# Kernel optimization log

Measured on AMD Instinct MI355X. Metric: run time of the kernel, lower is better.

Reference implementation:

```python
import jax, jax.numpy as jnp
import numpy as np


def setup_inputs() -> dict:
    key = jax.random.key(0)
    k1, k2, k3, k4 = jax.random.split(key, 4)
    N, F, E = 131072, 512, 256
    x = jax.random.normal(k1, (N, F), dtype=jnp.float32)
    W = jax.random.normal(k2, (E, F), dtype=jnp.float32) * 0.05  # stacked weak-classifier weights
    b = jax.random.normal(k3, (E,), dtype=jnp.float32) * 0.05
    alphas = jax.random.normal(k4, (E,), dtype=jnp.float32)
    return {"x": x, "W": W, "b": b, "alphas": alphas}


def reference(x, W, b, alphas):
    # Fused version of the per-estimator Python loop:
    # per estimator e: pred_e = round(sigmoid(x @ W[e] + b[e])) in {0,1}
    logits = jnp.einsum('nf,ef->ne', x, W) + b              # [N, E]
    preds = jnp.round(jax.nn.sigmoid(logits))               # [N, E], half-to-even like torch.round
    # original casts each (alpha * pred) term to long (trunc toward zero) before accumulating
    terms = jnp.trunc(alphas[None, :] * preds)              # [N, E]
    acc = jnp.sum(terms, axis=1)                            # [N]
    return jnp.sign(acc)
```

## Files before the change

kernel.cpp:

```cpp
#include <hip/hip_runtime.h>
#include <math.h>


#define BM 128
#define BN 128
#define BK 16
#define TAU 2e-4f
#define F_DIM 512

__device__ __attribute__((noinline)) bool exact_pred(const float* __restrict__ xr,
                                                     const float* __restrict__ wr,
                                                     float bv) {
    double s = (double)bv;
    for (int k = 0; k < F_DIM; ++k)
        s = fma((double)xr[k], (double)wr[k], s);
    return s > 0.0;
}

__global__ __launch_bounds__(256)
void ada_fused(const float* __restrict__ x, const float* __restrict__ W,
               const float* __restrict__ bias, const float* __restrict__ alphas,
               float* __restrict__ out) {
    __shared__ float xs[BK][BM];
    __shared__ float wsh[BK][BN];
    __shared__ int   rowacc[BM];
    __shared__ int   se[256];
    __shared__ float st[256];
    __shared__ float sb[256];
    __shared__ int   wcnt[4];

    const int tid = threadIdx.x;
    const int n0  = blockIdx.x * BM;

    se[tid] = 0; st[tid] = 0.0f; sb[tid] = 0.0f;
    if (tid < BM) rowacc[tid] = 0;
    __syncthreads();

    const float t = truncf(alphas[tid]);
    const bool flag = (t != 0.0f);
    const unsigned long long mask = __ballot(flag);
    const int lane = tid & 63, wv = tid >> 6;
    if (lane == 0) wcnt[wv] = __popcll(mask);
    __syncthreads();
    int off = 0;
    #pragma unroll
    for (int w = 0; w < 4; ++w)
        if (w < wv) off += wcnt[w];
    const int M = wcnt[0] + wcnt[1] + wcnt[2] + wcnt[3];
    if (flag) {
        const int slot = off + __popcll(mask & ((1ull << lane) - 1ull));
        se[slot] = tid;
        st[slot] = t;
        sb[slot] = bias[tid];
    }
    __syncthreads();

    const int ttx = tid & 15, tty = tid >> 4;
    const int row0 = ttx * 8, col0 = tty * 8;
    const int lr = tid >> 1;
    const int lk = (tid & 1) * 8;

    for (int cb = 0; cb < M; cb += BN) {
        const bool active = (cb + col0) < M;
        const int serow = se[cb + lr];
        const float4* xp = (const float4*)(x + (size_t)(n0 + lr) * F_DIM + lk);
        const float4* wp = (const float4*)(W + (size_t)serow * F_DIM + lk);

        float acc[8][8];
        #pragma unroll
        for (int r = 0; r < 8; ++r)
            #pragma unroll
            for (int c = 0; c < 8; ++c) acc[r][c] = 0.0f;

        for (int k0 = 0; k0 < F_DIM; k0 += BK) {
            const float4 xa = xp[0], xb = xp[1];
            const float4 wa = wp[0], wb = wp[1];
            xp += BK / 4; wp += BK / 4;
            __syncthreads();
            xs[lk + 0][lr] = xa.x; xs[lk + 1][lr] = xa.y;
            xs[lk + 2][lr] = xa.z; xs[lk + 3][lr] = xa.w;
            xs[lk + 4][lr] = xb.x; xs[lk + 5][lr] = xb.y;
            xs[lk + 6][lr] = xb.z; xs[lk + 7][lr] = xb.w;
            wsh[lk + 0][lr] = wa.x; wsh[lk + 1][lr] = wa.y;
            wsh[lk + 2][lr] = wa.z; wsh[lk + 3][lr] = wa.w;
            wsh[lk + 4][lr] = wb.x; wsh[lk + 5][lr] = wb.y;
            wsh[lk + 6][lr] = wb.z; wsh[lk + 7][lr] = wb.w;
            __syncthreads();
            if (active) {
                #pragma unroll
                for (int kk = 0; kk < BK; ++kk) {
                    float a[8], w8[8];
                    *(float4*)&a[0]  = *(const float4*)&xs[kk][row0];
                    *(float4*)&a[4]  = *(const float4*)&xs[kk][row0 + 4];
                    *(float4*)&w8[0] = *(const float4*)&wsh[kk][col0];
                    *(float4*)&w8[4] = *(const float4*)&wsh[kk][col0 + 4];
                    #pragma unroll
                    for (int r = 0; r < 8; ++r)
                        #pragma unroll
                        for (int c = 0; c < 8; ++c)
                            acc[r][c] = fmaf(a[r], w8[c], acc[r][c]);
                }
            }
        }

        if (active) {
            int partial[8];
            #pragma unroll
            for (int r = 0; r < 8; ++r) partial[r] = 0;
            #pragma unroll
            for (int c = 0; c < 8; ++c) {
                const int j = cb + col0 + c;
                const float tv = st[j];
                if (tv != 0.0f) {
                    const float bv = sb[j];
                    const int e = se[j];
                    #pragma unroll
                    for (int r = 0; r < 8; ++r) {
                        const float logit = acc[r][c] + bv;
                        bool pred = (logit > 0.0f);
                        if (fabsf(logit) < TAU) {
                            pred = exact_pred(x + (size_t)(n0 + row0 + r) * F_DIM,
                                              W + (size_t)e * F_DIM, bv);
                        }
                        if (pred) partial[r] += (int)tv;
                    }
                }
            }
            #pragma unroll
            for (int r = 0; r < 8; ++r)
                if (partial[r] != 0) atomicAdd(&rowacc[row0 + r], partial[r]);
        }
    }

    __syncthreads();
    if (tid < BM) {
        const int a = rowacc[tid];
        out[n0 + tid] = (a > 0) ? 1.0f : (a < 0 ? -1.0f : 0.0f);
    }
}

extern "C" void kernel_launch(void* const* d_in, const int* in_sizes, int n_in,
                              void* d_out, int out_size, void* d_ws, size_t ws_size,
                              hipStream_t stream) {
    const float* x      = (const float*)d_in[0];
    const float* W      = (const float*)d_in[1];
    const float* bias   = (const float*)d_in[2];
    const float* alphas = (const float*)d_in[3];
    float* out = (float*)d_out;

    const int n = in_sizes[0] / F_DIM;
    const int nblocks = n / BM;

    ada_fused<<<dim3(nblocks), dim3(256), 0, stream>>>(x, W, bias, alphas, out);
}
```

Baseline: 508.2 us.

## Replace FP32 SIMT GEMM with split-bf16 MFMA and register-level row reduction

Swaps the scalar FP32 outer-product GEMM for bf16 MFMA 16x16x32 instructions. Each FP32 value is split into hi/lo bf16 parts and three MFMAs are accumulated to get near-FP32 accuracy. Other changes: BK goes to 32, the exact-check threshold widens to 1e-3, the shared-memory row atomics give way to wave shuffles, and the double-precision fallback is unrolled with four accumulators. The aim is to use matrix cores on this compute-bound GEMM. The cost is the per-tile hi/lo conversion work, and the wider threshold may trigger more slow exact fallbacks.

```diff
diff --git a/kernel.cpp b/kernel.cpp
--- a/kernel.cpp
+++ b/kernel.cpp
@@ -2,140 +2,220 @@
 #include <math.h>
 
 
-#define BM 128
-#define BN 128
-#define BK 16
-#define TAU 2e-4f
 #define F_DIM 512
+#define BM    128
+#define BK    32
+#define NTMAX 8
+#define KPAD  40
+#define TAU   1e-3f
+
+typedef float f32x4  __attribute__((ext_vector_type(4)));
+typedef short bf16x8 __attribute__((ext_vector_type(8)));
+typedef unsigned short u16x4 __attribute__((ext_vector_type(4)));
+
+__device__ inline unsigned short bf16_rne(float v) {
+    unsigned u = __float_as_uint(v);
+    u += 0x7FFFu + ((u >> 16) & 1u);
+    return (unsigned short)(u >> 16);
+}
+__device__ inline float bf16_to_f32(unsigned short h) {
+    return __uint_as_float(((unsigned)h) << 16);
+}
 
 __device__ __attribute__((noinline)) bool exact_pred(const float* __restrict__ xr,
                                                      const float* __restrict__ wr,
                                                      float bv) {
-    double s = (double)bv;
-    for (int k = 0; k < F_DIM; ++k)
-        s = fma((double)xr[k], (double)wr[k], s);
+    double s0 = 0.0, s1 = 0.0, s2 = 0.0, s3 = 0.0;
+    for (int k = 0; k < F_DIM; k += 4) {
+        s0 = fma((double)xr[k + 0], (double)wr[k + 0], s0);
+        s1 = fma((double)xr[k + 1], (double)wr[k + 1], s1);
+        s2 = fma((double)xr[k + 2], (double)wr[k + 2], s2);
+        s3 = fma((double)xr[k + 3], (double)wr[k + 3], s3);
+    }
+    double s = ((s0 + s1) + (s2 + s3)) + (double)bv;
     return s > 0.0;
 }
 
-__global__ __launch_bounds__(256)
-void ada_fused(const float* __restrict__ x, const float* __restrict__ W,
-               const float* __restrict__ bias, const float* __restrict__ alphas,
-               float* __restrict__ out) {
-    __shared__ float xs[BK][BM];
-    __shared__ float wsh[BK][BN];
-    __shared__ int   rowacc[BM];
-    __shared__ int   se[256];
-    __shared__ float st[256];
-    __shared__ float sb[256];
+__global__ __launch_bounds__(256, 3)
+void ada_mfma(const float* __restrict__ x, const float* __restrict__ W,
+              const float* __restrict__ bias, const float* __restrict__ alphas,
+              float* __restrict__ out) {
+    __shared__ unsigned short xs_hi[BM][KPAD], xs_lo[BM][KPAD];
+    __shared__ unsigned short wh[128][KPAD],  wl[128][KPAD];
+    __shared__ int   se[272];
+    __shared__ float st[272];
+    __shared__ float sb[272];
     __shared__ int   wcnt[4];
 
     const int tid = threadIdx.x;
     const int n0  = blockIdx.x * BM;
 
     se[tid] = 0; st[tid] = 0.0f; sb[tid] = 0.0f;
-    if (tid < BM) rowacc[tid] = 0;
+    if (tid < 16) { se[256 + tid] = 0; st[256 + tid] = 0.0f; sb[256 + tid] = 0.0f; }
     __syncthreads();
-
     const float t = truncf(alphas[tid]);
     const bool flag = (t != 0.0f);
-    const unsigned long long mask = __ballot(flag);
-    const int lane = tid & 63, wv = tid >> 6;
-    if (lane == 0) wcnt[wv] = __popcll(mask);
+    const unsigned long long m64 = __ballot(flag);
+    const int lane = tid & 63, wvi = tid >> 6;
+    if (lane == 0) wcnt[wvi] = __popcll(m64);
     __syncthreads();
     int off = 0;
     #pragma unroll
-    for (int w = 0; w < 4; ++w)
-        if (w < wv) off += wcnt[w];
+    for (int w = 0; w < 4; ++w) if (w < wvi) off += wcnt[w];
     const int M = wcnt[0] + wcnt[1] + wcnt[2] + wcnt[3];
     if (flag) {
-        const int slot = off + __popcll(mask & ((1ull << lane) - 1ull));
-        se[slot] = tid;
-        st[slot] = t;
-        sb[slot] = bias[tid];
+        const int slot = off + __popcll(m64 & ((1ull << lane) - 1ull));
+        se[slot] = tid; st[slot] = t; sb[slot] = bias[tid];
     }
     __syncthreads();
 
-    const int ttx = tid & 15, tty = tid >> 4;
-    const int row0 = ttx * 8, col0 = tty * 8;
-    const int lr = tid >> 1;
-    const int lk = (tid & 1) * 8;
-
-    for (int cb = 0; cb < M; cb += BN) {
-        const bool active = (cb + col0) < M;
-        const int serow = se[cb + lr];
-        const float4* xp = (const float4*)(x + (size_t)(n0 + lr) * F_DIM + lk);
-        const float4* wp = (const float4*)(W + (size_t)serow * F_DIM + lk);
-
-        float acc[8][8];
-        #pragma unroll
-        for (int r = 0; r < 8; ++r)
-            #pragma unroll
-            for (int c = 0; c < 8; ++c) acc[r][c] = 0.0f;
+    const int sr   = tid >> 3;
+    const int sc   = (tid & 7) * 4;
+    const int quad = (tid >> 4) & 3;
+    const int l15  = tid & 15;
+    const int rw   = (tid >> 6) * 32;
+
+    const float* xp = x + (size_t)(n0 + sr) * F_DIM + sc;
+
+    int part[2][4];
+    #pragma unroll
+    for (int mt = 0; mt < 2; ++mt)
+        #pragma unroll
+        for (int r = 0; r < 4; ++r) part[mt][r] = 0;
+
+    for (int cb = 0; cb < M; cb += 128) {
+        const int Mrem   = M - cb;
+        const int NT     = (Mrem + 15) >> 4 < NTMAX ? (Mrem + 15) >> 4 : NTMAX;
+        const int wstage = (NT + 1) >> 1;
+
+        const float* wp[4];
+        #pragma unroll
+        for (int i = 0; i < 4; ++i) {
+            const int e = se[cb + sr + i * 32];
+            wp[i] = W + (size_t)e * F_DIM + sc;
+        }
+
+        f32x4 acc[2][NTMAX];
+        #pragma unroll
+        for (int mt = 0; mt < 2; ++mt)
+            #pragma unroll
+            for (int nt = 0; nt < NTMAX; ++nt)
+                acc[mt][nt] = (f32x4){0.0f, 0.0f, 0.0f, 0.0f};
 
         for (int k0 = 0; k0 < F_DIM; k0 += BK) {
-            const float4 xa = xp[0], xb = xp[1];
-            const float4 wa = wp[0], wb = wp[1];
-            xp += BK / 4; wp += BK / 4;
+            float4 xv[4], wvv[4];
+            #pragma unroll
+            for (int i = 0; i < 4; ++i)
+                xv[i] = *(const float4*)(xp + (size_t)i * 32 * F_DIM + k0);
+            #pragma unroll
+            for (int i = 0; i < 4; ++i)
+                if (i < wstage) wvv[i] = *(const float4*)(wp[i] + k0);
+
             __syncthreads();
-            xs[lk + 0][lr] = xa.x; xs[lk + 1][lr] = xa.y;
-            xs[lk + 2][lr] = xa.z; xs[lk + 3][lr] = xa.w;
-            xs[lk + 4][lr] = xb.x; xs[lk + 5][lr] = xb.y;
-            xs[lk + 6][lr] = xb.z; xs[lk + 7][lr] = xb.w;
-            wsh[lk + 0][lr] = wa.x; wsh[lk + 1][lr] = wa.y;
-            wsh[lk + 2][lr] = wa.z; wsh[lk + 3][lr] = wa.w;
-            wsh[lk + 4][lr] = wb.x; wsh[lk + 5][lr] = wb.y;
-            wsh[lk + 6][lr] = wb.z; wsh[lk + 7][lr] = wb.w;
+
+            #pragma unroll
+            for (int i = 0; i < 4; ++i) {
+                const int r = sr + i * 32;
+                const float vv[4] = {xv[i].x, xv[i].y, xv[i].z, xv[i].w};
+                u16x4 hv, lv;
+                #pragma unroll
+                for (int j = 0; j < 4; ++j) {
+                    const unsigned short h = bf16_rne(vv[j]);
+                    hv[j] = h;
+                    lv[j] = bf16_rne(vv[j] - bf16_to_f32(h));
+                }
+                *(u16x4*)&xs_hi[r][sc] = hv;
+                *(u16x4*)&xs_lo[r][sc] = lv;
+            }
+            #pragma unroll
+            for (int i = 0; i < 4; ++i) {
+                if (i < wstage) {
+                    const int r = sr + i * 32;
+                    const float vv[4] = {wvv[i].x, wvv[i].y, wvv[i].z, wvv[i].w};
+                    u16x4 hv, lv;
+                    #pragma unroll
+                    for (int j = 0; j < 4; ++j) {
+                        const unsigned short h = bf16_rne(vv[j]);
+                        hv[j] = h;
+                        lv[j] = bf16_rne(vv[j] - bf16_to_f32(h));
+                    }
+                    *(u16x4*)&wh[r][sc] = hv;
+                    *(u16x4*)&wl[r][sc] = lv;
+                }
+            }
+
             __syncthreads();
-            if (active) {
-                #pragma unroll
-                for (int kk = 0; kk < BK; ++kk) {
-                    float a[8], w8[8];
-                    *(float4*)&a[0]  = *(const float4*)&xs[kk][row0];
-                    *(float4*)&a[4]  = *(const float4*)&xs[kk][row0 + 4];
-                    *(float4*)&w8[0] = *(const float4*)&wsh[kk][col0];
-                    *(float4*)&w8[4] = *(const float4*)&wsh[kk][col0 + 4];
+
+            bf16x8 ah[2], al[2];
+            #pragma unroll
+            for (int mt = 0; mt < 2; ++mt) {
+                ah[mt] = *(const bf16x8*)&xs_hi[rw + mt * 16 + l15][quad * 8];
+                al[mt] = *(const bf16x8*)&xs_lo[rw + mt * 16 + l15][quad * 8];
+            }
+            #pragma unroll
+            for (int nt = 0; nt < NTMAX; ++nt) {
+                if (nt < NT) {
+                    const bf16x8 bh = *(const bf16x8*)&wh[nt * 16 + l15][quad * 8];
+                    const bf16x8 bl = *(const bf16x8*)&wl[nt * 16 + l15][quad * 8];
                     #pragma unroll
-                    for (int r = 0; r < 8; ++r)
+                    for (int mt = 0; mt < 2; ++mt) {
+                        acc[mt][nt] = __builtin_amdgcn_mfma_f32_16x16x32_bf16(ah[mt], bh, acc[mt][nt], 0, 0, 0);
+                        acc[mt][nt] = __builtin_amdgcn_mfma_f32_16x16x32_bf16(al[mt], bh, acc[mt][nt], 0, 0, 0);
+                        acc[mt][nt] = __builtin_amdgcn_mfma_f32_16x16x32_bf16(ah[mt], bl, acc[mt][nt], 0, 0, 0);
+                    }
+                }
+            }
+        }
+
+        #pragma unroll
+        for (int nt = 0; nt < NTMAX; ++nt) {
+            if (nt < NT) {
+                const int col = cb + nt * 16 + l15;
+                const float tv = st[col];
+                if (tv != 0.0f) {
+                    const float bv = sb[col];
+                    const int it = (int)tv;
+                    #pragma unroll
+                    for (int mt = 0; mt < 2; ++mt) {
                         #pragma unroll
-                        for (int c = 0; c < 8; ++c)
-                            acc[r][c] = fmaf(a[r], w8[c], acc[r][c]);
-                }
-            }
-        }
-
-        if (active) {
-            int partial[8];
-            #pragma unroll
-            for (int r = 0; r < 8; ++r) partial[r] = 0;
-            #pragma unroll
-            for (int c = 0; c < 8; ++c) {
-                const int j = cb + col0 + c;
-                const float tv = st[j];
-                if (tv != 0.0f) {
-                    const float bv = sb[j];
-                    const int e = se[j];
-                    #pragma unroll
-                    for (int r = 0; r < 8; ++r) {
-                        const float logit = acc[r][c] + bv;
-                        bool pred = (logit > 0.0f);
-                        if (fabsf(logit) < TAU) {
-                            pred = exact_pred(x + (size_t)(n0 + row0 + r) * F_DIM,
-                                              W + (size_t)e * F_DIM, bv);
+                        for (int r = 0; r < 4; ++r) {
+                            const float logit = acc[mt][nt][r] + bv;
+                            bool pred = (logit > 0.0f);
+                            if (fabsf(logit) < TAU) {
+                                const int row = rw + mt * 16 + quad * 4 + r;
+                                pred = exact_pred(x + (size_t)(n0 + row) * F_DIM,
+                                                  W + (size_t)se[col] * F_DIM, bv);
+                            }
+                            if (pred) part[mt][r] += it;
                         }
-                        if (pred) partial[r] += (int)tv;
                     }
                 }
             }
-            #pragma unroll
-            for (int r = 0; r < 8; ++r)
-                if (partial[r] != 0) atomicAdd(&rowacc[row0 + r], partial[r]);
-        }
-    }
-
-    __syncthreads();
-    if (tid < BM) {
-        const int a = rowacc[tid];
-        out[n0 + tid] = (a > 0) ? 1.0f : (a < 0 ? -1.0f : 0.0f);
+        }
+    }
+
+    #pragma unroll
+    for (int mt = 0; mt < 2; ++mt) {
+        #pragma unroll
+        for (int r = 0; r < 4; ++r) {
+            int v = part[mt][r];
+            v += __shfl_xor(v, 1);
+            v += __shfl_xor(v, 2);
+            v += __shfl_xor(v, 4);
+            v += __shfl_xor(v, 8);
+            part[mt][r] = v;
+        }
+    }
+    if (l15 == 0) {
+        #pragma unroll
+        for (int mt = 0; mt < 2; ++mt) {
+            float4 o;
+            o.x = (part[mt][0] > 0) ? 1.0f : (part[mt][0] < 0 ? -1.0f : 0.0f);
+            o.y = (part[mt][1] > 0) ? 1.0f : (part[mt][1] < 0 ? -1.0f : 0.0f);
+            o.z = (part[mt][2] > 0) ? 1.0f : (part[mt][2] < 0 ? -1.0f : 0.0f);
+            o.w = (part[mt][3] > 0) ? 1.0f : (part[mt][3] < 0 ? -1.0f : 0.0f);
+            *(float4*)(out + n0 + rw + mt * 16 + quad * 4) = o;
+        }
     }
 }
 
@@ -151,5 +231,5 @@
     const int n = in_sizes[0] / F_DIM;
     const int nblocks = n / BM;
 
-    ada_fused<<<dim3(nblocks), dim3(256), 0, stream>>>(x, W, bias, alphas, out);
-}
+    ada_mfma<<<dim3(nblocks), dim3(256), 0, stream>>>(x, W, bias, alphas, out);
+}
```

Result: faster. 495.2 us (-2.5%).
